# Kernel optimization log

Measured on AMD Instinct MI355X. Metric: run time of the kernel, lower is better.

Reference implementation:

```python
import math
import jax, jax.numpy as jnp
import numpy as np


def _median_torch_style(t):
    # torch: flatten, sort, average the middle two if even length
    s = jnp.sort(t.ravel())
    L = s.shape[0]
    if L % 2 == 0:
        m = L // 2
        return (s[m - 1] + s[m]) * 0.5
    else:
        return s[(L - 1) // 2]


def setup_inputs() -> dict:
    key = jax.random.key(0)
    kx, ky = jax.random.split(key)
    N, M, d = 4096, 4096, 64
    X = jax.random.normal(kx, (N, d), dtype=jnp.float32)
    Y = jax.random.normal(ky, (M, d), dtype=jnp.float32)
    return {"X": X, "Y": Y}


def reference(X, Y):
    # (same math as diag(XX)/diag(YY) in the original, without the wasted GEMMs)
    XY = X @ Y.T                                  # [N, M]
    x_sq = jnp.sum(X * X, axis=1)                 # [N] == diag(X X^T)
    y_sq = jnp.sum(Y * Y, axis=1)                 # [M] == diag(Y Y^T)
    dnorm2 = -2.0 * XY + x_sq[:, None] + y_sq[None, :]

    # h is None in this configuration -> median bandwidth heuristic
    med = _median_torch_style(jax.lax.stop_gradient(dnorm2))
    h = med / (2.0 * jnp.float32(math.log(X.shape[0])))
    gamma = 1.0 / (2.0 * h)
    K_XY = jnp.exp(-gamma * dnorm2)
    return K_XY
```

## Files before the change

kernel.cpp:

```cpp
#include <hip/hip_runtime.h>
#include <math.h>

#define NROWS 4096
#define DDIM  64
#define NBINS 2048
#define NSHARD 8
#define HIST_W    0.25f
#define HIST_INVW 4.0f


typedef __attribute__((ext_vector_type(8))) short short8;
typedef __attribute__((ext_vector_type(4))) float f32x4;

__device__ inline unsigned short f2bf(float f) {
    unsigned u = __builtin_bit_cast(unsigned, f);
    u += 0x7FFFu + ((u >> 16) & 1u);
    return (unsigned short)(u >> 16);
}
__device__ inline float bf2f(unsigned short h) {
    unsigned u = ((unsigned)h) << 16;
    return __builtin_bit_cast(float, u);
}

__global__ void prep_kernel(const float* __restrict__ X, const float* __restrict__ Y,
                            unsigned short* __restrict__ Xh, unsigned short* __restrict__ Xl,
                            unsigned short* __restrict__ Yh, unsigned short* __restrict__ Yl,
                            float* __restrict__ x_sq, float* __restrict__ y_sq,
                            unsigned* __restrict__ hist8, unsigned* __restrict__ ticket,
                            unsigned* __restrict__ flag) {
    int gid = blockIdx.x * blockDim.x + threadIdx.x;
    if (gid < NSHARD * NBINS) hist8[gid] = 0u;
    if (gid == 0) { *ticket = 0u; *flag = 0u; }
    int row = gid >> 3, kb = gid & 7;
    int r = (row < NROWS) ? row : row - NROWS;
    const float* src = ((row < NROWS) ? X : Y) + (size_t)r * DDIM + kb * 8;
    unsigned short* dh = (row < NROWS) ? Xh : Yh;
    unsigned short* dl = (row < NROWS) ? Xl : Yl;
    float* sq = (row < NROWS) ? x_sq : y_sq;

    float4 a = *(const float4*)src;
    float4 b = *(const float4*)(src + 4);
    float v[8] = {a.x, a.y, a.z, a.w, b.x, b.y, b.z, b.w};
    short8 vh, vl;
    float s = 0.f;
#pragma unroll
    for (int j = 0; j < 8; ++j) {
        s = fmaf(v[j], v[j], s);
        unsigned short h = f2bf(v[j]);
        vh[j] = (short)h;
        vl[j] = (short)f2bf(v[j] - bf2f(h));
    }
    s += __shfl_xor(s, 1);
    s += __shfl_xor(s, 2);
    s += __shfl_xor(s, 4);
    if (kb == 0) sq[r] = s;
    size_t o = ((size_t)(r >> 4) * 8 + kb) * 128 + (size_t)(r & 15) * 8;
    *(short8*)(dh + o) = vh;
    *(short8*)(dl + o) = vl;
}

template <typename F>
__device__ inline void compute_tile_hh(const unsigned short* __restrict__ Xh,
                                       const unsigned short* __restrict__ Yh,
                                       int i0, int j0, size_t la, F&& body) {
    const int pa0 = i0 >> 4, pb0 = j0 >> 4;
    short8 fxh[8], fyh[8];
#pragma unroll
    for (int kh = 0; kh < 2; ++kh)
#pragma unroll
        for (int g = 0; g < 4; ++g) {
            fxh[kh * 4 + g] = *(const short8*)(Xh + ((size_t)(pa0 + g) * 8 + kh * 4) * 128 + la);
            fyh[kh * 4 + g] = *(const short8*)(Yh + ((size_t)(pb0 + g) * 8 + kh * 4) * 128 + la);
        }
    f32x4 acc[4][4];
#pragma unroll
    for (int r = 0; r < 4; ++r)
#pragma unroll
        for (int c = 0; c < 4; ++c) acc[r][c] = (f32x4){0.f, 0.f, 0.f, 0.f};
#pragma unroll
    for (int kh = 0; kh < 2; ++kh)
#pragma unroll
        for (int r = 0; r < 4; ++r)
#pragma unroll
            for (int c = 0; c < 4; ++c)
                acc[r][c] = __builtin_amdgcn_mfma_f32_16x16x32_bf16(fxh[kh * 4 + r], fyh[kh * 4 + c], acc[r][c], 0, 0, 0);
    body(acc);
}

__launch_bounds__(256, 2)
__global__ void hist_kernel(const unsigned short* __restrict__ Xh,
                            const unsigned short* __restrict__ Yh,
                            const float* __restrict__ x_sq, const float* __restrict__ y_sq,
                            unsigned* __restrict__ hist8) {
    __shared__ unsigned lhist[NBINS];
    const int t    = threadIdx.x;
    const int wave = t >> 6;
    const int lane = t & 63;
    const int fr = lane & 15;
    const int rb = (lane >> 4) * 4;
    const size_t la = (size_t)lane * 8;
    const int i0 = blockIdx.y * 128 + (wave >> 1) * 64;
    const int j0 = blockIdx.x * 1024 + (blockIdx.y & 7) * 128 + (wave & 1) * 64;

#pragma unroll
    for (int i = 0; i < NBINS / 256; ++i) lhist[t + i * 256] = 0u;
    __syncthreads();

    float xsv[4][4];
#pragma unroll
    for (int r = 0; r < 4; ++r)
#pragma unroll
        for (int q = 0; q < 4; ++q) xsv[r][q] = x_sq[i0 + r * 16 + rb + q];
    float ysv[4];
#pragma unroll
    for (int c = 0; c < 4; ++c) ysv[c] = y_sq[j0 + c * 16 + fr];

    compute_tile_hh(Xh, Yh, i0, j0, la, [&](f32x4 (&acc)[4][4]) {
#pragma unroll
        for (int r = 0; r < 4; ++r)
#pragma unroll
            for (int q = 0; q < 4; ++q) {
                float xs = xsv[r][q];
#pragma unroll
                for (int c = 0; c < 4; ++c) {
                    float dv = fmaf(-2.f, acc[r][c][q], xs + ysv[c]);
                    int idx = (int)(dv * HIST_INVW);
                    idx = idx < 0 ? 0 : (idx > NBINS - 1 ? NBINS - 1 : idx);
                    atomicAdd(&lhist[idx], 1u);
                }
            }
    });
    __syncthreads();
    unsigned* dst = hist8 + (size_t)((blockIdx.y * gridDim.x + blockIdx.x) & (NSHARD - 1)) * NBINS;
#pragma unroll
    for (int i = 0; i < NBINS / 256; ++i) {
        unsigned cv = lhist[t + i * 256];
        if (cv) atomicAdd(&dst[t + i * 256], cv);
    }
}

__launch_bounds__(256, 2)
__global__ void write_kernel(const unsigned short* __restrict__ Xh, const unsigned short* __restrict__ Xl,
                             const unsigned short* __restrict__ Yh, const unsigned short* __restrict__ Yl,
                             const float* __restrict__ x_sq, const float* __restrict__ y_sq,
                             const unsigned* __restrict__ hist8, unsigned* __restrict__ ticket,
                             unsigned* __restrict__ flag, unsigned* __restrict__ params,
                             float* __restrict__ out) {
    __shared__ float T[4][64][68];
    __shared__ int s_red;
    __shared__ float s_cc;
    const int t    = threadIdx.x;
    const int wave = t >> 6;
    const int lane = t & 63;
    const int fr = lane & 15;
    const int rb = (lane >> 4) * 4;
    const size_t la = (size_t)lane * 8;
    const int i0  = blockIdx.y * 128 + (wave >> 1) * 64;
    const int j0b = blockIdx.x * 256 + (wave & 1) * 64;

    if (t == 0) s_red = (atomicAdd(ticket, 1u) == 0u);
    __syncthreads();

    if (s_red) {
        unsigned* cnt  = (unsigned*)&T[0][0][0];
        unsigned* tsum = cnt + NBINS;
        float*    vmed = (float*)(tsum + 256);
        unsigned s = 0;
#pragma unroll
        for (int i = 0; i < NBINS / 256; ++i) {
            unsigned b = t * (NBINS / 256) + i;
            unsigned cv = 0;
#pragma unroll
            for (int sd = 0; sd < NSHARD; ++sd)
                cv += hist8[sd * NBINS + b];
            cnt[b] = cv;
            s += cv;
        }
        tsum[t] = s;
        __syncthreads();
        for (int off = 1; off < 256; off <<= 1) {
            unsigned v = (t >= off) ? tsum[t - off] : 0u;
            __syncthreads();
            tsum[t] += v;
            __syncthreads();
        }
        unsigned cum = (t == 0) ? 0u : tsum[t - 1];
        unsigned total = tsum[255];
        const unsigned K2 = total >> 1;
        const unsigned K1 = K2 - 1u + (total & 1u);
        for (int i = 0; i < NBINS / 256; ++i) {
            int b = t * (NBINS / 256) + i;
            unsigned cv = cnt[b];
            if (cv) {
                if (K1 >= cum && (K1 - cum) < cv)
                    vmed[0] = ((float)b + ((float)(K1 - cum) + 0.5f) / (float)cv) * HIST_W;
                if (K2 >= cum && (K2 - cum) < cv)
                    vmed[1] = ((float)b + ((float)(K2 - cum) + 0.5f) / (float)cv) * HIST_W;
            }
            cum += cv;
        }
        __syncthreads();
        if (t == 0) {
            double med   = 0.5 * ((double)vmed[0] + (double)vmed[1]);
            double gamma = 8.317766166719343 / med;
            float  c     = (float)(-gamma * 1.4426950408889634);
            atomicExch(params, __builtin_bit_cast(unsigned, c));
            __threadfence();
            atomicExch(flag, 1u);
        }
        __syncthreads();
    }

    const int pa0 = i0 >> 4;

    float xsv[4][4];
#pragma unroll
    for (int r = 0; r < 4; ++r)
#pragma unroll
        for (int q = 0; q < 4; ++q) xsv[r][q] = x_sq[i0 + r * 16 + rb + q];

    short8 fxh[8], fxl[8];
#pragma unroll
    for (int kh = 0; kh < 2; ++kh)
#pragma unroll
        for (int g = 0; g < 4; ++g) {
            const size_t ao = ((size_t)(pa0 + g) * 8 + kh * 4) * 128 + la;
            fxh[kh * 4 + g] = *(const short8*)(Xh + ao);
            fxl[kh * 4 + g] = *(const short8*)(Xl + ao);
        }

#pragma unroll 1
    for (int jt = 0; jt < 2; ++jt) {
        const int j0 = j0b + jt * 128;
        const int pb0 = j0 >> 4;

        short8 fyh[8], fyl[8];
#pragma unroll
        for (int kh = 0; kh < 2; ++kh)
#pragma unroll
            for (int g = 0; g < 4; ++g) {
                const size_t bo = ((size_t)(pb0 + g) * 8 + kh * 4) * 128 + la;
                fyh[kh * 4 + g] = *(const short8*)(Yh + bo);
                fyl[kh * 4 + g] = *(const short8*)(Yl + bo);
            }

        f32x4 acc[4][4];
#pragma unroll
        for (int r = 0; r < 4; ++r)
#pragma unroll
            for (int c = 0; c < 4; ++c) acc[r][c] = (f32x4){0.f, 0.f, 0.f, 0.f};
#pragma unroll
        for (int kh = 0; kh < 2; ++kh)
#pragma unroll
            for (int r = 0; r < 4; ++r)
#pragma unroll
                for (int c = 0; c < 4; ++c) {
                    acc[r][c] = __builtin_amdgcn_mfma_f32_16x16x32_bf16(fxh[kh * 4 + r], fyh[kh * 4 + c], acc[r][c], 0, 0, 0);
                    acc[r][c] = __builtin_amdgcn_mfma_f32_16x16x32_bf16(fxl[kh * 4 + r], fyh[kh * 4 + c], acc[r][c], 0, 0, 0);
                    acc[r][c] = __builtin_amdgcn_mfma_f32_16x16x32_bf16(fxh[kh * 4 + r], fyl[kh * 4 + c], acc[r][c], 0, 0, 0);
                    acc[r][c] = __builtin_amdgcn_mfma_f32_16x16x32_bf16(fxl[kh * 4 + r], fyl[kh * 4 + c], acc[r][c], 0, 0, 0);
                }

        if (jt == 0) {
            if (t == 0) {
                while (atomicAdd(flag, 0u) == 0u) __builtin_amdgcn_s_sleep(8);
                s_cc = __builtin_bit_cast(float, atomicAdd(params, 0u));
            }
            __syncthreads();
        }
        const float cc = s_cc;

        float ysv[4];
#pragma unroll
        for (int c = 0; c < 4; ++c) ysv[c] = y_sq[j0 + c * 16 + fr];

        float* Tw = &T[wave][0][0];
#pragma unroll
        for (int r = 0; r < 4; ++r)
#pragma unroll
            for (int c = 0; c < 4; ++c)
#pragma unroll
                for (int q = 0; q < 4; ++q) {
                    float dv = fmaf(-2.f, acc[r][c][q], xsv[r][q] + ysv[c]);
                    Tw[(r * 16 + rb + q) * 68 + c * 16 + fr] = __builtin_amdgcn_exp2f(cc * dv);
                }
#pragma unroll
        for (int ii = 0; ii < 16; ++ii) {
            int row = ii * 4 + (lane >> 4);
            f32x4 v = *(const f32x4*)&Tw[row * 68 + fr * 4];
            f32x4* po = (f32x4*)(out + (size_t)(i0 + row) * NROWS + j0 + fr * 4);
            __builtin_nontemporal_store(v, po);
        }
    }
}

extern "C" void kernel_launch(void* const* d_in, const int* in_sizes, int n_in,
                              void* d_out, int out_size, void* d_ws, size_t ws_size,
                              hipStream_t stream) {
    const float* X = (const float*)d_in[0];
    const float* Y = (const float*)d_in[1];
    float* out = (float*)d_out;

    unsigned* hist8    = (unsigned*)d_ws;
    float* x_sq        = (float*)((char*)d_ws + 65536);
    float* y_sq        = (float*)((char*)d_ws + 81920);
    unsigned* params   = (unsigned*)((char*)d_ws + 98304);
    unsigned* ticket   = (unsigned*)((char*)d_ws + 98308);
    unsigned* flag     = (unsigned*)((char*)d_ws + 98312);
    unsigned short* Xh = (unsigned short*)((char*)d_ws + 131072);
    unsigned short* Xl = Xh + (size_t)NROWS * DDIM;
    unsigned short* Yh = Xl + (size_t)NROWS * DDIM;
    unsigned short* Yl = Yh + (size_t)NROWS * DDIM;

    prep_kernel<<<256, 256, 0, stream>>>(X, Y, Xh, Xl, Yh, Yl, x_sq, y_sq, hist8, ticket, flag);
    hist_kernel<<<dim3(4, 32), 256, 0, stream>>>(Xh, Yh, x_sq, y_sq, hist8);
    write_kernel<<<dim3(16, 32), 256, 0, stream>>>(Xh, Xl, Yh, Yl, x_sq, y_sq,
                                                   hist8, ticket, flag, params, out);
}
```

Before: 35.22 us.

## Unroll write-kernel tile loop to prefetch second Y tile, remap prep threads

The write kernel's two-iteration tile loop is manually unrolled. The second tile's Y fragments are now loaded before the first tile's results are stored, so those global loads overlap the output stores and the next MFMA batch. The flag wait is hoisted out of the loop. The prep kernel is remapped so each thread converts two 8-element chunks of one row within a 16-row panel, reducing squared norms with lane shuffles, and launches half as many blocks. The extra live registers for the prefetched fragments may raise register pressure.

```diff
diff --git a/kernel.cpp b/kernel.cpp
--- a/kernel.cpp
+++ b/kernel.cpp
@@ -28,35 +28,44 @@
                             float* __restrict__ x_sq, float* __restrict__ y_sq,
                             unsigned* __restrict__ hist8, unsigned* __restrict__ ticket,
                             unsigned* __restrict__ flag) {
-    int gid = blockIdx.x * blockDim.x + threadIdx.x;
+    const int t   = threadIdx.x;
+    const int gid = blockIdx.x * 256 + t;
     if (gid < NSHARD * NBINS) hist8[gid] = 0u;
     if (gid == 0) { *ticket = 0u; *flag = 0u; }
-    int row = gid >> 3, kb = gid & 7;
-    int r = (row < NROWS) ? row : row - NROWS;
-    const float* src = ((row < NROWS) ? X : Y) + (size_t)r * DDIM + kb * 8;
-    unsigned short* dh = (row < NROWS) ? Xh : Yh;
-    unsigned short* dl = (row < NROWS) ? Xl : Yl;
-    float* sq = (row < NROWS) ? x_sq : y_sq;
-
-    float4 a = *(const float4*)src;
-    float4 b = *(const float4*)(src + 4);
-    float v[8] = {a.x, a.y, a.z, a.w, b.x, b.y, b.z, b.w};
-    short8 vh, vl;
+
+    const int fr    = t & 15;
+    const int kb0   = (t >> 4) & 3;
+    const int panel = gid >> 6;
+    const int pm    = panel & 255;
+    const int prow  = pm * 16 + fr;
+
+    const float* src = ((panel < 256) ? X : Y) + (size_t)prow * DDIM;
+    unsigned short* dh = (panel < 256) ? Xh : Yh;
+    unsigned short* dl = (panel < 256) ? Xl : Yl;
+    float* sq = (panel < 256) ? x_sq : y_sq;
+
     float s = 0.f;
 #pragma unroll
-    for (int j = 0; j < 8; ++j) {
-        s = fmaf(v[j], v[j], s);
-        unsigned short h = f2bf(v[j]);
-        vh[j] = (short)h;
-        vl[j] = (short)f2bf(v[j] - bf2f(h));
-    }
-    s += __shfl_xor(s, 1);
-    s += __shfl_xor(s, 2);
-    s += __shfl_xor(s, 4);
-    if (kb == 0) sq[r] = s;
-    size_t o = ((size_t)(r >> 4) * 8 + kb) * 128 + (size_t)(r & 15) * 8;
-    *(short8*)(dh + o) = vh;
-    *(short8*)(dl + o) = vl;
+    for (int h = 0; h < 2; ++h) {
+        const int kb = kb0 + 4 * h;
+        float4 a = *(const float4*)(src + kb * 8);
+        float4 b = *(const float4*)(src + kb * 8 + 4);
+        float v[8] = {a.x, a.y, a.z, a.w, b.x, b.y, b.z, b.w};
+        short8 vh, vl;
+#pragma unroll
+        for (int j = 0; j < 8; ++j) {
+            s = fmaf(v[j], v[j], s);
+            unsigned short hh = f2bf(v[j]);
+            vh[j] = (short)hh;
+            vl[j] = (short)f2bf(v[j] - bf2f(hh));
+        }
+        size_t o = ((size_t)pm * 8 + kb) * 128 + (size_t)fr * 8;
+        *(short8*)(dh + o) = vh;
+        *(short8*)(dl + o) = vl;
+    }
+    s += __shfl_xor(s, 16);
+    s += __shfl_xor(s, 32);
+    if (kb0 == 0) sq[prow] = s;
 }
 
 template <typename F>
@@ -157,6 +166,8 @@
     const size_t la = (size_t)lane * 8;
     const int i0  = blockIdx.y * 128 + (wave >> 1) * 64;
     const int j0b = blockIdx.x * 256 + (wave & 1) * 64;
+    const int j1  = j0b;
+    const int j2  = j0b + 128;
 
     if (t == 0) s_red = (atomicAdd(ticket, 1u) == 0u);
     __syncthreads();
@@ -212,7 +223,6 @@
     }
 
     const int pa0 = i0 >> 4;
-
     float xsv[4][4];
 #pragma unroll
     for (int r = 0; r < 4; ++r)
@@ -229,11 +239,9 @@
             fxl[kh * 4 + g] = *(const short8*)(Xl + ao);
         }
 
-#pragma unroll 1
-    for (int jt = 0; jt < 2; ++jt) {
-        const int j0 = j0b + jt * 128;
-        const int pb0 = j0 >> 4;
-
+    f32x4 acc[4][4];
+    {
+        const int pb0 = j1 >> 4;
         short8 fyh[8], fyl[8];
 #pragma unroll
         for (int kh = 0; kh < 2; ++kh)
@@ -243,8 +251,6 @@
                 fyh[kh * 4 + g] = *(const short8*)(Yh + bo);
                 fyl[kh * 4 + g] = *(const short8*)(Yl + bo);
             }
-
-        f32x4 acc[4][4];
 #pragma unroll
         for (int r = 0; r < 4; ++r)
 #pragma unroll
@@ -260,21 +266,20 @@
                     acc[r][c] = __builtin_amdgcn_mfma_f32_16x16x32_bf16(fxh[kh * 4 + r], fyl[kh * 4 + c], acc[r][c], 0, 0, 0);
                     acc[r][c] = __builtin_amdgcn_mfma_f32_16x16x32_bf16(fxl[kh * 4 + r], fyl[kh * 4 + c], acc[r][c], 0, 0, 0);
                 }
-
-        if (jt == 0) {
-            if (t == 0) {
-                while (atomicAdd(flag, 0u) == 0u) __builtin_amdgcn_s_sleep(8);
-                s_cc = __builtin_bit_cast(float, atomicAdd(params, 0u));
-            }
-            __syncthreads();
-        }
-        const float cc = s_cc;
-
+    }
+
+    if (t == 0) {
+        while (atomicAdd(flag, 0u) == 0u) __builtin_amdgcn_s_sleep(8);
+        s_cc = __builtin_bit_cast(float, atomicAdd(params, 0u));
+    }
+    __syncthreads();
+    const float cc = s_cc;
+
+    float* Tw = &T[wave][0][0];
+    {
         float ysv[4];
 #pragma unroll
-        for (int c = 0; c < 4; ++c) ysv[c] = y_sq[j0 + c * 16 + fr];
-
-        float* Tw = &T[wave][0][0];
+        for (int c = 0; c < 4; ++c) ysv[c] = y_sq[j1 + c * 16 + fr];
 #pragma unroll
         for (int r = 0; r < 4; ++r)
 #pragma unroll
@@ -284,11 +289,62 @@
                     float dv = fmaf(-2.f, acc[r][c][q], xsv[r][q] + ysv[c]);
                     Tw[(r * 16 + rb + q) * 68 + c * 16 + fr] = __builtin_amdgcn_exp2f(cc * dv);
                 }
+    }
+
+    short8 gyh[8], gyl[8];
+    {
+        const int pb0 = j2 >> 4;
+#pragma unroll
+        for (int kh = 0; kh < 2; ++kh)
+#pragma unroll
+            for (int g = 0; g < 4; ++g) {
+                const size_t bo = ((size_t)(pb0 + g) * 8 + kh * 4) * 128 + la;
+                gyh[kh * 4 + g] = *(const short8*)(Yh + bo);
+                gyl[kh * 4 + g] = *(const short8*)(Yl + bo);
+            }
+    }
+
+#pragma unroll
+    for (int ii = 0; ii < 16; ++ii) {
+        int row = ii * 4 + (lane >> 4);
+        f32x4 v = *(const f32x4*)&Tw[row * 68 + fr * 4];
+        f32x4* po = (f32x4*)(out + (size_t)(i0 + row) * NROWS + j1 + fr * 4);
+        __builtin_nontemporal_store(v, po);
+    }
+
+#pragma unroll
+    for (int r = 0; r < 4; ++r)
+#pragma unroll
+        for (int c = 0; c < 4; ++c) acc[r][c] = (f32x4){0.f, 0.f, 0.f, 0.f};
+#pragma unroll
+    for (int kh = 0; kh < 2; ++kh)
+#pragma unroll
+        for (int r = 0; r < 4; ++r)
+#pragma unroll
+            for (int c = 0; c < 4; ++c) {
+                acc[r][c] = __builtin_amdgcn_mfma_f32_16x16x32_bf16(fxh[kh * 4 + r], gyh[kh * 4 + c], acc[r][c], 0, 0, 0);
+                acc[r][c] = __builtin_amdgcn_mfma_f32_16x16x32_bf16(fxl[kh * 4 + r], gyh[kh * 4 + c], acc[r][c], 0, 0, 0);
+                acc[r][c] = __builtin_amdgcn_mfma_f32_16x16x32_bf16(fxh[kh * 4 + r], gyl[kh * 4 + c], acc[r][c], 0, 0, 0);
+                acc[r][c] = __builtin_amdgcn_mfma_f32_16x16x32_bf16(fxl[kh * 4 + r], gyl[kh * 4 + c], acc[r][c], 0, 0, 0);
+            }
+    {
+        float ysv[4];
+#pragma unroll
+        for (int c = 0; c < 4; ++c) ysv[c] = y_sq[j2 + c * 16 + fr];
+#pragma unroll
+        for (int r = 0; r < 4; ++r)
+#pragma unroll
+            for (int c = 0; c < 4; ++c)
+#pragma unroll
+                for (int q = 0; q < 4; ++q) {
+                    float dv = fmaf(-2.f, acc[r][c][q], xsv[r][q] + ysv[c]);
+                    Tw[(r * 16 + rb + q) * 68 + c * 16 + fr] = __builtin_amdgcn_exp2f(cc * dv);
+                }
 #pragma unroll
         for (int ii = 0; ii < 16; ++ii) {
             int row = ii * 4 + (lane >> 4);
             f32x4 v = *(const f32x4*)&Tw[row * 68 + fr * 4];
-            f32x4* po = (f32x4*)(out + (size_t)(i0 + row) * NROWS + j0 + fr * 4);
+            f32x4* po = (f32x4*)(out + (size_t)(i0 + row) * NROWS + j2 + fr * 4);
             __builtin_nontemporal_store(v, po);
         }
     }
@@ -312,7 +368,7 @@
     unsigned short* Yh = Xl + (size_t)NROWS * DDIM;
     unsigned short* Yl = Yh + (size_t)NROWS * DDIM;
 
-    prep_kernel<<<256, 256, 0, stream>>>(X, Y, Xh, Xl, Yh, Yl, x_sq, y_sq, hist8, ticket, flag);
+    prep_kernel<<<128, 256, 0, stream>>>(X, Y, Xh, Xl, Yh, Yl, x_sq, y_sq, hist8, ticket, flag);
     hist_kernel<<<dim3(4, 32), 256, 0, stream>>>(Xh, Yh, x_sq, y_sq, hist8);
     write_kernel<<<dim3(16, 32), 256, 0, stream>>>(Xh, Xl, Yh, Yl, x_sq, y_sq,
                                                    hist8, ticket, flag, params, out);
```

Measured after the change: 36.63 us. 1.04x slower.
